# Optimization experiments

Hardware: AMD Instinct MI355X
Metric: run time of the kernel (lower is better)

## Reference

```python
import jax, jax.numpy as jnp
import numpy as np

B, L, D, H = 2, 256, 256, 4
DH = D // H  # 64


def setup_inputs() -> dict:
    key = jax.random.key(0)
    ks = jax.random.split(key, 20)
    inp = {
        "q": jax.random.normal(ks[0], (B, L, D), jnp.float32),
        "k": jax.random.normal(ks[1], (B, L, D), jnp.float32),
        "v": jax.random.normal(ks[2], (B, L, D), jnp.float32),
        "attn_mask": jnp.zeros((L, L), jnp.float32),  # nonzero => masked
        "key_padding_mask": jnp.zeros((B, L), bool),
        "pitch_rel": jax.random.normal(ks[3], (B, L, L, D), jnp.float32),
        "dur_rel": jax.random.normal(ks[4], (B, L, L, D), jnp.float32),
    }
    scale = 1.0 / np.sqrt(D)
    names = ["Wq", "Wk", "Wv", "fc", "pr", "dr"]
    for i, n in enumerate(names):
        inp[n + "_w"] = jax.random.normal(ks[5 + 2 * i], (D, D), jnp.float32) * scale
        inp[n + "_b"] = jax.random.normal(ks[6 + 2 * i], (D,), jnp.float32) * 0.01
    return inp


def _linear(x, w, b):
    # torch nn.Linear: y = x @ W^T + b
    return jnp.matmul(x, w.T) + b


def reference(q, k, v, attn_mask, key_padding_mask, pitch_rel, dur_rel,
              Wq_w, Wq_b, Wk_w, Wk_b, Wv_w, Wv_b, fc_w, fc_b,
              pr_w, pr_b, dr_w, dr_b):
    Bq, Lq, Dm = q.shape
    Lk = k.shape[1]
    # project and split heads -> (B, H, L, DH)
    def heads(x, w, b):
        return _linear(x, w, b).reshape(Bq, -1, H, DH).transpose(0, 2, 1, 3)
    qh, kh, vh = heads(q, Wq_w, Wq_b), heads(k, Wk_w, Wk_b), heads(v, Wv_w, Wv_b)

    # content scores: (B, H, Lq, Lk)
    logits = jnp.einsum("bhid,bhjd->bhij", qh, kh)

    # relative pitch bias: pitch_rel (B, Lq, Lk, D) -> (B, Lq, Lk, H, DH)
    pr = _linear(pitch_rel, pr_w, pr_b).reshape(Bq, Lq, Lk, H, DH)
    logits = logits + jnp.einsum("bhid,bijhd->bhij", qh, pr)

    dr = _linear(dur_rel, dr_w, dr_b).reshape(Bq, Lq, Lk, H, DH)
    logits = logits + jnp.einsum("bhid,bijhd->bhij", qh, dr)

    logits = logits / np.sqrt(DH)

    # mask: key_padding_mask broadcast over the QUERY axis (as in source),
    # attn_mask nonzero => masked
    mask = jnp.logical_or(key_padding_mask[:, None, :, None],
                          (attn_mask != 0)[None, None, :, :])
    logits = jnp.where(mask, jnp.float32(-9e15), logits)

    attn = jax.nn.softmax(logits, axis=-1)  # (B, H, Lq, Lk)
    out = jnp.einsum("bhij,bhjd->bhid", attn, vh)  # (B, H, Lq, DH)
    out = out.transpose(0, 2, 1, 3).reshape(Bq, Lq, Dm)
    out = _linear(out, fc_w, fc_b)  # dropout is identity in eval mode
    return out, attn
```

## Files before the change

kernel.cpp:

```cpp
#include <hip/hip_runtime.h>
#include <math.h>


__global__ __launch_bounds__(256) void k_transpose(const float* __restrict__ in,
                                                   float* __restrict__ out) {
  __shared__ float t[32][33];
  int bx = blockIdx.x & 7, by = blockIdx.x >> 3;
  int x = threadIdx.x & 31, y0 = threadIdx.x >> 5;
#pragma unroll
  for (int yy = 0; yy < 32; yy += 8)
    t[yy + y0][x] = in[(size_t)(by * 32 + yy + y0) * 256 + bx * 32 + x];
  __syncthreads();
#pragma unroll
  for (int yy = 0; yy < 32; yy += 8)
    out[(size_t)(bx * 32 + yy + y0) * 256 + by * 32 + x] = t[x][yy + y0];
}

__global__ __launch_bounds__(256) void k_proj(
    const float* __restrict__ q, const float* __restrict__ k_, const float* __restrict__ v,
    const float* __restrict__ Wq, const float* __restrict__ Bq,
    const float* __restrict__ Wk, const float* __restrict__ Bk,
    const float* __restrict__ Wv, const float* __restrict__ Bv,
    float* __restrict__ qh, float* __restrict__ kh, float* __restrict__ vh) {
  int blk = blockIdx.x;
  int m = blk >> 5;
  int r = blk & 31;
  int b = r >> 4, it = (r >> 2) & 3, ot = r & 3;
  const float* X = (m == 0) ? q : (m == 1) ? k_ : v;
  const float* W = (m == 0) ? Wq : (m == 1) ? Wk : Wv;
  const float* Bs = (m == 0) ? Bq : (m == 1) ? Bk : Bv;
  float* OUT = (m == 0) ? qh : (m == 1) ? kh : vh;
  const float scale = (m == 0) ? 0.125f : 1.0f;

  __shared__ float xs[64][33];
  __shared__ float ws[64][33];
  int tid = threadIdx.x;
  int ti = tid >> 4, to = tid & 15;
  int lr = tid >> 2, lc = (tid & 3) * 8;
  float acc[4][4] = {};

  for (int k0 = 0; k0 < 256; k0 += 32) {
    float4 a0 = *(const float4*)(X + (size_t)(b * 256 + it * 64 + lr) * 256 + k0 + lc);
    float4 a1 = *(const float4*)(X + (size_t)(b * 256 + it * 64 + lr) * 256 + k0 + lc + 4);
    xs[lr][lc + 0] = a0.x; xs[lr][lc + 1] = a0.y; xs[lr][lc + 2] = a0.z; xs[lr][lc + 3] = a0.w;
    xs[lr][lc + 4] = a1.x; xs[lr][lc + 5] = a1.y; xs[lr][lc + 6] = a1.z; xs[lr][lc + 7] = a1.w;
    float4 w0 = *(const float4*)(W + (size_t)(ot * 64 + lr) * 256 + k0 + lc);
    float4 w1 = *(const float4*)(W + (size_t)(ot * 64 + lr) * 256 + k0 + lc + 4);
    ws[lr][lc + 0] = w0.x; ws[lr][lc + 1] = w0.y; ws[lr][lc + 2] = w0.z; ws[lr][lc + 3] = w0.w;
    ws[lr][lc + 4] = w1.x; ws[lr][lc + 5] = w1.y; ws[lr][lc + 6] = w1.z; ws[lr][lc + 7] = w1.w;
    __syncthreads();
#pragma unroll
    for (int kk = 0; kk < 32; ++kk) {
      float xv0 = xs[ti * 4 + 0][kk], xv1 = xs[ti * 4 + 1][kk];
      float xv2 = xs[ti * 4 + 2][kk], xv3 = xs[ti * 4 + 3][kk];
      float wv0 = ws[0 * 16 + to][kk], wv1 = ws[1 * 16 + to][kk];
      float wv2 = ws[2 * 16 + to][kk], wv3 = ws[3 * 16 + to][kk];
      acc[0][0] += xv0 * wv0; acc[0][1] += xv0 * wv1; acc[0][2] += xv0 * wv2; acc[0][3] += xv0 * wv3;
      acc[1][0] += xv1 * wv0; acc[1][1] += xv1 * wv1; acc[1][2] += xv1 * wv2; acc[1][3] += xv1 * wv3;
      acc[2][0] += xv2 * wv0; acc[2][1] += xv2 * wv1; acc[2][2] += xv2 * wv2; acc[2][3] += xv2 * wv3;
      acc[3][0] += xv3 * wv0; acc[3][1] += xv3 * wv1; acc[3][2] += xv3 * wv2; acc[3][3] += xv3 * wv3;
    }
    __syncthreads();
  }
#pragma unroll
  for (int ii = 0; ii < 4; ++ii)
#pragma unroll
    for (int oo = 0; oo < 4; ++oo) {
      int i = it * 64 + ti * 4 + ii;
      int dd = oo * 16 + to;
      OUT[(size_t)((b * 4 + ot) * 256 + i) * 64 + dd] = (acc[ii][oo] + Bs[ot * 64 + dd]) * scale;
    }
}

__global__ __launch_bounds__(256) void k_qprdr(
    const float* __restrict__ qh, const float* __restrict__ prw,
    const float* __restrict__ drw, float* __restrict__ qpr, float* __restrict__ qdr) {
  int blk = blockIdx.x;
  int t = blk >> 7;
  int r2 = blk & 127;
  int rt = r2 >> 2, et = r2 & 3;
  const float* W = t ? drw : prw;
  float* OUT = t ? qdr : qpr;
  int h = (rt >> 2) & 3;

  __shared__ float xs[64][33];
  __shared__ float ws2[32][64];
  int tid = threadIdx.x;
  int ti = tid >> 4, to = tid & 15;
  float acc[4][4] = {};

  for (int k0 = 0; k0 < 64; k0 += 32) {
    int lr = tid >> 2, lc = (tid & 3) * 8;
    float4 a0 = *(const float4*)(qh + (size_t)(rt * 64 + lr) * 64 + k0 + lc);
    float4 a1 = *(const float4*)(qh + (size_t)(rt * 64 + lr) * 64 + k0 + lc + 4);
    xs[lr][lc + 0] = a0.x; xs[lr][lc + 1] = a0.y; xs[lr][lc + 2] = a0.z; xs[lr][lc + 3] = a0.w;
    xs[lr][lc + 4] = a1.x; xs[lr][lc + 5] = a1.y; xs[lr][lc + 6] = a1.z; xs[lr][lc + 7] = a1.w;
    int wr = tid >> 3, wc = (tid & 7) * 8;
    float4 w0 = *(const float4*)(W + (size_t)(h * 64 + k0 + wr) * 256 + et * 64 + wc);
    float4 w1 = *(const float4*)(W + (size_t)(h * 64 + k0 + wr) * 256 + et * 64 + wc + 4);
    ws2[wr][wc + 0] = w0.x; ws2[wr][wc + 1] = w0.y; ws2[wr][wc + 2] = w0.z; ws2[wr][wc + 3] = w0.w;
    ws2[wr][wc + 4] = w1.x; ws2[wr][wc + 5] = w1.y; ws2[wr][wc + 6] = w1.z; ws2[wr][wc + 7] = w1.w;
    __syncthreads();
#pragma unroll
    for (int kk = 0; kk < 32; ++kk) {
      float xv0 = xs[ti * 4 + 0][kk], xv1 = xs[ti * 4 + 1][kk];
      float xv2 = xs[ti * 4 + 2][kk], xv3 = xs[ti * 4 + 3][kk];
      float wv0 = ws2[kk][0 * 16 + to], wv1 = ws2[kk][1 * 16 + to];
      float wv2 = ws2[kk][2 * 16 + to], wv3 = ws2[kk][3 * 16 + to];
      acc[0][0] += xv0 * wv0; acc[0][1] += xv0 * wv1; acc[0][2] += xv0 * wv2; acc[0][3] += xv0 * wv3;
      acc[1][0] += xv1 * wv0; acc[1][1] += xv1 * wv1; acc[1][2] += xv1 * wv2; acc[1][3] += xv1 * wv3;
      acc[2][0] += xv2 * wv0; acc[2][1] += xv2 * wv1; acc[2][2] += xv2 * wv2; acc[2][3] += xv2 * wv3;
      acc[3][0] += xv3 * wv0; acc[3][1] += xv3 * wv1; acc[3][2] += xv3 * wv2; acc[3][3] += xv3 * wv3;
    }
    __syncthreads();
  }
#pragma unroll
  for (int ii = 0; ii < 4; ++ii)
#pragma unroll
    for (int oo = 0; oo < 4; ++oo)
      OUT[(size_t)(rt * 64 + ti * 4 + ii) * 256 + et * 64 + oo * 16 + to] = acc[ii][oo];
}

__global__ __launch_bounds__(256) void k_qk(const float* __restrict__ qh,
                                            const float* __restrict__ kh,
                                            float* __restrict__ qk) {
  int blk = blockIdx.x;
  int bh = blk >> 4, it = (blk >> 2) & 3, jt = blk & 3;
  __shared__ float xs[64][33];
  __shared__ float ys[64][33];
  int tid = threadIdx.x;
  int ti = tid >> 4, to = tid & 15;
  float acc[4][4] = {};

  for (int k0 = 0; k0 < 64; k0 += 32) {
    int lr = tid >> 2, lc = (tid & 3) * 8;
    float4 a0 = *(const float4*)(qh + (size_t)(bh * 256 + it * 64 + lr) * 64 + k0 + lc);
    float4 a1 = *(const float4*)(qh + (size_t)(bh * 256 + it * 64 + lr) * 64 + k0 + lc + 4);
    xs[lr][lc + 0] = a0.x; xs[lr][lc + 1] = a0.y; xs[lr][lc + 2] = a0.z; xs[lr][lc + 3] = a0.w;
    xs[lr][lc + 4] = a1.x; xs[lr][lc + 5] = a1.y; xs[lr][lc + 6] = a1.z; xs[lr][lc + 7] = a1.w;
    float4 b0 = *(const float4*)(kh + (size_t)(bh * 256 + jt * 64 + lr) * 64 + k0 + lc);
    float4 b1 = *(const float4*)(kh + (size_t)(bh * 256 + jt * 64 + lr) * 64 + k0 + lc + 4);
    ys[lr][lc + 0] = b0.x; ys[lr][lc + 1] = b0.y; ys[lr][lc + 2] = b0.z; ys[lr][lc + 3] = b0.w;
    ys[lr][lc + 4] = b1.x; ys[lr][lc + 5] = b1.y; ys[lr][lc + 6] = b1.z; ys[lr][lc + 7] = b1.w;
    __syncthreads();
#pragma unroll
    for (int kk = 0; kk < 32; ++kk) {
      float xv0 = xs[ti * 4 + 0][kk], xv1 = xs[ti * 4 + 1][kk];
      float xv2 = xs[ti * 4 + 2][kk], xv3 = xs[ti * 4 + 3][kk];
      float wv0 = ys[0 * 16 + to][kk], wv1 = ys[1 * 16 + to][kk];
      float wv2 = ys[2 * 16 + to][kk], wv3 = ys[3 * 16 + to][kk];
      acc[0][0] += xv0 * wv0; acc[0][1] += xv0 * wv1; acc[0][2] += xv0 * wv2; acc[0][3] += xv0 * wv3;
      acc[1][0] += xv1 * wv0; acc[1][1] += xv1 * wv1; acc[1][2] += xv1 * wv2; acc[1][3] += xv1 * wv3;
      acc[2][0] += xv2 * wv0; acc[2][1] += xv2 * wv1; acc[2][2] += xv2 * wv2; acc[2][3] += xv2 * wv3;
      acc[3][0] += xv3 * wv0; acc[3][1] += xv3 * wv1; acc[3][2] += xv3 * wv2; acc[3][3] += xv3 * wv3;
    }
    __syncthreads();
  }
#pragma unroll
  for (int ii = 0; ii < 4; ++ii)
#pragma unroll
    for (int jj = 0; jj < 4; ++jj)
      qk[(size_t)(bh * 256 + it * 64 + ti * 4 + ii) * 256 + jt * 64 + jj * 16 + to] = acc[ii][jj];
}

__global__ __launch_bounds__(256, 3) void k_bias(
    const float* __restrict__ pitch, const float* __restrict__ dur,
    const float* __restrict__ qpr, const float* __restrict__ qdr,
    const float* __restrict__ amask, const unsigned char* __restrict__ kpm,
    float* __restrict__ attn) {
  int blk = blockIdx.x;
  int jc = blk & 7;
  int bi = blk >> 3;
  int b = bi >> 8, i = bi & 255;
  int tid = threadIdx.x, w = tid >> 6, l = tid & 63;
  int jb = jc * 32 + w * 8;

  __shared__ float red[4][8][4][65];

  float4 qp[4], qd[4];
#pragma unroll
  for (int h = 0; h < 4; ++h) {
    qp[h] = *(const float4*)(qpr + (size_t)((b * 4 + h) * 256 + i) * 256 + 4 * l);
    qd[h] = *(const float4*)(qdr + (size_t)((b * 4 + h) * 256 + i) * 256 + 4 * l);
  }

  int p = l & 31;
  int jj_o = p >> 2, h_o = p & 3;
  int jabs = jb + jj_o;
  size_t orow = (size_t)((b * 4 + h_o) * 256 + i) * 256 + jabs;
  float qkreg = attn[orow];
  bool maskreg = (kpm[b * 256 + i] != 0) || (amask[(size_t)i * 256 + jabs] != 0.f);

  const float4* prow = (const float4*)(pitch + ((size_t)(b * 256 + i) * 256 + jb) * 256);
  const float4* drow = (const float4*)(dur + ((size_t)(b * 256 + i) * 256 + jb) * 256);

  float4 P[8], D[8];
#pragma unroll
  for (int g = 0; g < 8; ++g) P[g] = prow[(size_t)g * 64 + l];
#pragma unroll
  for (int g = 0; g < 8; ++g) D[g] = drow[(size_t)g * 64 + l];

  float acc[8][4];
#pragma unroll
  for (int jj = 0; jj < 8; ++jj)
#pragma unroll
    for (int h = 0; h < 4; ++h)
      acc[jj][h] = P[jj].x * qp[h].x + P[jj].y * qp[h].y + P[jj].z * qp[h].z + P[jj].w * qp[h].w
                 + D[jj].x * qd[h].x + D[jj].y * qd[h].y + D[jj].z * qd[h].z + D[jj].w * qd[h].w;

#pragma unroll
  for (int jj = 0; jj < 8; ++jj)
#pragma unroll
    for (int h = 0; h < 4; ++h)
      red[w][jj][h][l] = acc[jj][h];

  int half = l >> 5;
  const float* rrow = &red[w][jj_o][h_o][0];
  float x = 0.f;
#pragma unroll
  for (int c = 0; c < 32; ++c) x += rrow[half * 32 + c];
  x += __shfl_xor(x, 32);

  if (l < 32) {
    float val = qkreg + x;
    if (maskreg) val = -9e15f;
    attn[orow] = val;
  }
}

__global__ __launch_bounds__(256) void k_pv_fc(
    float* __restrict__ attn, const float* __restrict__ vh,
    const float* __restrict__ fcT, const float* __restrict__ fcb,
    float* __restrict__ out) {
  int b = blockIdx.x >> 8, i = blockIdx.x & 255;
  int tid = threadIdx.x;
  int h = tid >> 6, l = tid & 63;

  __shared__ float arow[4][256];
  __shared__ float pre[256];

  float* rowp = attn + (size_t)((b * 4 + h) * 256 + i) * 256;
  float4 v4 = *(float4*)(rowp + 4 * l);
  float mx = fmaxf(fmaxf(v4.x, v4.y), fmaxf(v4.z, v4.w));
#pragma unroll
  for (int m = 1; m <= 32; m <<= 1) mx = fmaxf(mx, __shfl_xor(mx, m));
  float e0 = __expf(v4.x - mx), e1 = __expf(v4.y - mx);
  float e2 = __expf(v4.z - mx), e3 = __expf(v4.w - mx);
  float sm = e0 + e1 + e2 + e3;
#pragma unroll
  for (int m = 1; m <= 32; m <<= 1) sm += __shfl_xor(sm, m);
  float inv = 1.0f / sm;
  float4 a4 = make_float4(e0 * inv, e1 * inv, e2 * inv, e3 * inv);
  *(float4*)(rowp + 4 * l) = a4;
  *(float4*)&arow[h][4 * l] = a4;
  __syncthreads();

  float acc = 0.f;
  const float* vbase = vh + (size_t)(b * 4 + h) * 256 * 64 + l;
#pragma unroll 4
  for (int jj = 0; jj < 256; ++jj) acc += arow[h][jj] * vbase[(size_t)jj * 64];
  pre[tid] = acc;
  __syncthreads();

  float acc2 = fcb[tid];
#pragma unroll 4
  for (int c = 0; c < 256; ++c) acc2 += pre[c] * fcT[(size_t)c * 256 + tid];
  out[(size_t)(b * 256 + i) * 256 + tid] = acc2;
}

extern "C" void kernel_launch(void* const* d_in, const int* in_sizes, int n_in,
                              void* d_out, int out_size, void* d_ws, size_t ws_size,
                              hipStream_t stream) {
  (void)in_sizes; (void)n_in; (void)out_size; (void)ws_size;
  const float* q = (const float*)d_in[0];
  const float* k = (const float*)d_in[1];
  const float* v = (const float*)d_in[2];
  const float* amask = (const float*)d_in[3];
  const unsigned char* kpm = (const unsigned char*)d_in[4];
  const float* pitch = (const float*)d_in[5];
  const float* dur = (const float*)d_in[6];
  const float* Wq = (const float*)d_in[7];
  const float* Bq = (const float*)d_in[8];
  const float* Wk = (const float*)d_in[9];
  const float* Bk = (const float*)d_in[10];
  const float* Wv = (const float*)d_in[11];
  const float* Bv = (const float*)d_in[12];
  const float* fcw = (const float*)d_in[13];
  const float* fcb = (const float*)d_in[14];
  const float* prw = (const float*)d_in[15];
  const float* drw = (const float*)d_in[17];

  float* out = (float*)d_out;
  float* attn = out + 2 * 256 * 256;

  float* wsf = (float*)d_ws;
  float* qh = wsf;
  float* kh = qh + 131072;
  float* vh = kh + 131072;
  float* qpr = vh + 131072;
  float* qdr = qpr + 524288;
  float* fcT = qdr + 524288;

  k_transpose<<<64, 256, 0, stream>>>(fcw, fcT);
  k_proj<<<96, 256, 0, stream>>>(q, k, v, Wq, Bq, Wk, Bk, Wv, Bv, qh, kh, vh);
  k_qprdr<<<256, 256, 0, stream>>>(qh, prw, drw, qpr, qdr);
  k_qk<<<128, 256, 0, stream>>>(qh, kh, attn);
  k_bias<<<4096, 256, 0, stream>>>(pitch, dur, qpr, qdr, amask, kpm, attn);
  k_pv_fc<<<512, 256, 0, stream>>>(attn, vh, fcT, fcb, out);
}
```

Measured before the change: 117.0 us.

## Double-buffer pitch/dur loads in k_bias with one block per query row

The relative-bias kernel now gives each block a whole query row, so each wave covers 64 keys in 8 groups instead of one group of 8 keys. Register loads for the next group are issued before the current group is reduced and stored, overlapping memory traffic with compute. The large pitch/dur streams are read with nontemporal loads to avoid polluting the cache. The grid shrinks from 4096 to 512 blocks and the launch bound drops to 2 blocks per unit, trading occupancy for more registers and in-wave latency hiding.

```diff
diff --git a/kernel.cpp b/kernel.cpp
--- a/kernel.cpp
+++ b/kernel.cpp
@@ -1,6 +1,13 @@
 #include <hip/hip_runtime.h>
 #include <math.h>
 
+
+typedef float nfloat4 __attribute__((ext_vector_type(4)));
+
+static __device__ __forceinline__ float4 ntload4(const float4* p) {
+  nfloat4 r = __builtin_nontemporal_load((const nfloat4*)p);
+  return make_float4(r.x, r.y, r.z, r.w);
+}
 
 __global__ __launch_bounds__(256) void k_transpose(const float* __restrict__ in,
                                                    float* __restrict__ out) {
@@ -163,17 +170,15 @@
       qk[(size_t)(bh * 256 + it * 64 + ti * 4 + ii) * 256 + jt * 64 + jj * 16 + to] = acc[ii][jj];
 }
 
-__global__ __launch_bounds__(256, 3) void k_bias(
+__global__ __launch_bounds__(256, 2) void k_bias(
     const float* __restrict__ pitch, const float* __restrict__ dur,
     const float* __restrict__ qpr, const float* __restrict__ qdr,
     const float* __restrict__ amask, const unsigned char* __restrict__ kpm,
     float* __restrict__ attn) {
-  int blk = blockIdx.x;
-  int jc = blk & 7;
-  int bi = blk >> 3;
+  int bi = blockIdx.x;
   int b = bi >> 8, i = bi & 255;
   int tid = threadIdx.x, w = tid >> 6, l = tid & 63;
-  int jb = jc * 32 + w * 8;
+  int jbase = w * 64;
 
   __shared__ float red[4][8][4][65];
 
@@ -186,46 +191,64 @@
 
   int p = l & 31;
   int jj_o = p >> 2, h_o = p & 3;
-  int jabs = jb + jj_o;
-  size_t orow = (size_t)((b * 4 + h_o) * 256 + i) * 256 + jabs;
-  float qkreg = attn[orow];
-  bool maskreg = (kpm[b * 256 + i] != 0) || (amask[(size_t)i * 256 + jabs] != 0.f);
-
-  const float4* prow = (const float4*)(pitch + ((size_t)(b * 256 + i) * 256 + jb) * 256);
-  const float4* drow = (const float4*)(dur + ((size_t)(b * 256 + i) * 256 + jb) * 256);
-
-  float4 P[8], D[8];
-#pragma unroll
-  for (int g = 0; g < 8; ++g) P[g] = prow[(size_t)g * 64 + l];
-#pragma unroll
-  for (int g = 0; g < 8; ++g) D[g] = drow[(size_t)g * 64 + l];
-
-  float acc[8][4];
-#pragma unroll
-  for (int jj = 0; jj < 8; ++jj)
-#pragma unroll
-    for (int h = 0; h < 4; ++h)
-      acc[jj][h] = P[jj].x * qp[h].x + P[jj].y * qp[h].y + P[jj].z * qp[h].z + P[jj].w * qp[h].w
-                 + D[jj].x * qd[h].x + D[jj].y * qd[h].y + D[jj].z * qd[h].z + D[jj].w * qd[h].w;
-
-#pragma unroll
-  for (int jj = 0; jj < 8; ++jj)
-#pragma unroll
-    for (int h = 0; h < 4; ++h)
-      red[w][jj][h][l] = acc[jj][h];
-
-  int half = l >> 5;
-  const float* rrow = &red[w][jj_o][h_o][0];
-  float x = 0.f;
-#pragma unroll
-  for (int c = 0; c < 32; ++c) x += rrow[half * 32 + c];
-  x += __shfl_xor(x, 32);
-
-  if (l < 32) {
-    float val = qkreg + x;
-    if (maskreg) val = -9e15f;
-    attn[orow] = val;
-  }
+  size_t orow0 = (size_t)((b * 4 + h_o) * 256 + i) * 256 + jbase + jj_o;
+  bool rowm = kpm[b * 256 + i] != 0;
+  float qk8[8];
+  int mbits = 0;
+#pragma unroll
+  for (int g = 0; g < 8; ++g) {
+    qk8[g] = attn[orow0 + 8 * g];
+    if (rowm || amask[(size_t)i * 256 + jbase + g * 8 + jj_o] != 0.f) mbits |= (1 << g);
+  }
+
+  const float4* prow =
+      (const float4*)(pitch + (size_t)(b * 256 + i) * 65536) + (size_t)jbase * 64 + l;
+  const float4* drow =
+      (const float4*)(dur + (size_t)(b * 256 + i) * 65536) + (size_t)jbase * 64 + l;
+
+  float4 Pa[8], Da[8], Pb[8], Db[8];
+
+#define LOADG(PB, DB, g)                                  \
+  {                                                       \
+    _Pragma("unroll") for (int t = 0; t < 8; ++t) {       \
+      PB[t] = ntload4(prow + ((g) * 8 + t) * 64);         \
+      DB[t] = ntload4(drow + ((g) * 8 + t) * 64);         \
+    }                                                     \
+  }
+
+#define CSTORE(PB, DB, g)                                                       \
+  {                                                                             \
+    _Pragma("unroll") for (int t = 0; t < 8; ++t) {                             \
+      _Pragma("unroll") for (int h = 0; h < 4; ++h) {                           \
+        red[w][t][h][l] =                                                       \
+            PB[t].x * qp[h].x + PB[t].y * qp[h].y + PB[t].z * qp[h].z +         \
+            PB[t].w * qp[h].w + DB[t].x * qd[h].x + DB[t].y * qd[h].y +         \
+            DB[t].z * qd[h].z + DB[t].w * qd[h].w;                              \
+      }                                                                         \
+    }                                                                           \
+    float x = 0.f;                                                              \
+    {                                                                           \
+      const float* rr = &red[w][jj_o][h_o][(l >> 5) * 32];                      \
+      _Pragma("unroll 8") for (int c = 0; c < 32; ++c) x += rr[c];              \
+    }                                                                           \
+    x += __shfl_xor(x, 32);                                                     \
+    if (l < 32) {                                                               \
+      float val = qk8[g] + x;                                                   \
+      if (mbits & (1 << (g))) val = -9e15f;                                     \
+      attn[orow0 + 8 * (g)] = val;                                              \
+    }                                                                           \
+  }
+
+  LOADG(Pa, Da, 0);
+#pragma unroll
+  for (int gg = 0; gg < 4; ++gg) {
+    LOADG(Pb, Db, 2 * gg + 1);
+    CSTORE(Pa, Da, 2 * gg);
+    if (gg < 3) LOADG(Pa, Da, 2 * gg + 2);
+    CSTORE(Pb, Db, 2 * gg + 1);
+  }
+#undef LOADG
+#undef CSTORE
 }
 
 __global__ __launch_bounds__(256) void k_pv_fc(
@@ -305,6 +328,6 @@
   k_proj<<<96, 256, 0, stream>>>(q, k, v, Wq, Bq, Wk, Bk, Wv, Bv, qh, kh, vh);
   k_qprdr<<<256, 256, 0, stream>>>(qh, prw, drw, qpr, qdr);
   k_qk<<<128, 256, 0, stream>>>(qh, kh, attn);
-  k_bias<<<4096, 256, 0, stream>>>(pitch, dur, qpr, qdr, amask, kpm, attn);
+  k_bias<<<512, 256, 0, stream>>>(pitch, dur, qpr, qdr, amask, kpm, attn);
   k_pv_fc<<<512, 256, 0, stream>>>(attn, vh, fcT, fcb, out);
 }
```

New measurement: 120.7 us. 1.03x slower.

## Merge small kernels, restructure bias kernel for occupancy, move masking into softmax

Applied to the files above, without the earlier changes.

The transpose, q·pr/q·dr and QK kernels are folded into one launch that dispatches on block index, removing two launches. The bias kernel now writes the pitch/duration bias to a separate workspace buffer. It processes 64 keys per block in four groups, uses fewer registers and a smaller shared-memory reduction, and is bounded for 8 blocks per CU instead of 3. The QK add, masking and softmax are folded into the PV+FC kernel. The bias kernel keeps fewer loads in flight per thread in exchange for higher occupancy, and the new bias buffer adds an extra global write and read.

```diff
diff --git a/kernel.cpp b/kernel.cpp
--- a/kernel.cpp
+++ b/kernel.cpp
@@ -1,20 +1,6 @@
 #include <hip/hip_runtime.h>
 #include <math.h>
 
-
-__global__ __launch_bounds__(256) void k_transpose(const float* __restrict__ in,
-                                                   float* __restrict__ out) {
-  __shared__ float t[32][33];
-  int bx = blockIdx.x & 7, by = blockIdx.x >> 3;
-  int x = threadIdx.x & 31, y0 = threadIdx.x >> 5;
-#pragma unroll
-  for (int yy = 0; yy < 32; yy += 8)
-    t[yy + y0][x] = in[(size_t)(by * 32 + yy + y0) * 256 + bx * 32 + x];
-  __syncthreads();
-#pragma unroll
-  for (int yy = 0; yy < 32; yy += 8)
-    out[(size_t)(bx * 32 + yy + y0) * 256 + by * 32 + x] = t[x][yy + y0];
-}
 
 __global__ __launch_bounds__(256) void k_proj(
     const float* __restrict__ q, const float* __restrict__ k_, const float* __restrict__ v,
@@ -72,10 +58,9 @@
     }
 }
 
-__global__ __launch_bounds__(256) void k_qprdr(
-    const float* __restrict__ qh, const float* __restrict__ prw,
-    const float* __restrict__ drw, float* __restrict__ qpr, float* __restrict__ qdr) {
-  int blk = blockIdx.x;
+static __device__ void body_qprdr(int blk, const float* __restrict__ qh,
+                                  const float* __restrict__ prw, const float* __restrict__ drw,
+                                  float* __restrict__ qpr, float* __restrict__ qdr) {
   int t = blk >> 7;
   int r2 = blk & 127;
   int rt = r2 >> 2, et = r2 & 3;
@@ -121,10 +106,8 @@
       OUT[(size_t)(rt * 64 + ti * 4 + ii) * 256 + et * 64 + oo * 16 + to] = acc[ii][oo];
 }
 
-__global__ __launch_bounds__(256) void k_qk(const float* __restrict__ qh,
-                                            const float* __restrict__ kh,
-                                            float* __restrict__ qk) {
-  int blk = blockIdx.x;
+static __device__ void body_qk(int blk, const float* __restrict__ qh,
+                               const float* __restrict__ kh, float* __restrict__ qk) {
   int bh = blk >> 4, it = (blk >> 2) & 3, jt = blk & 3;
   __shared__ float xs[64][33];
   __shared__ float ys[64][33];
@@ -163,19 +146,43 @@
       qk[(size_t)(bh * 256 + it * 64 + ti * 4 + ii) * 256 + jt * 64 + jj * 16 + to] = acc[ii][jj];
 }
 
-__global__ __launch_bounds__(256, 3) void k_bias(
+static __device__ void body_transpose(int blk, const float* __restrict__ in,
+                                      float* __restrict__ out) {
+  __shared__ float t[32][33];
+  int bx = blk & 7, by = blk >> 3;
+  int x = threadIdx.x & 31, y0 = threadIdx.x >> 5;
+#pragma unroll
+  for (int yy = 0; yy < 32; yy += 8)
+    t[yy + y0][x] = in[(size_t)(by * 32 + yy + y0) * 256 + bx * 32 + x];
+  __syncthreads();
+#pragma unroll
+  for (int yy = 0; yy < 32; yy += 8)
+    out[(size_t)(bx * 32 + yy + y0) * 256 + by * 32 + x] = t[x][yy + y0];
+}
+
+__global__ __launch_bounds__(256) void k_mid(
+    const float* __restrict__ qh, const float* __restrict__ kh,
+    const float* __restrict__ prw, const float* __restrict__ drw,
+    float* __restrict__ qpr, float* __restrict__ qdr, float* __restrict__ qk,
+    const float* __restrict__ fcw, float* __restrict__ fcT) {
+  int blk = blockIdx.x;
+  if (blk < 256) body_qprdr(blk, qh, prw, drw, qpr, qdr);
+  else if (blk < 384) body_qk(blk - 256, qh, kh, qk);
+  else body_transpose(blk - 384, fcw, fcT);
+}
+
+__global__ __launch_bounds__(256, 8) void k_bias(
     const float* __restrict__ pitch, const float* __restrict__ dur,
     const float* __restrict__ qpr, const float* __restrict__ qdr,
-    const float* __restrict__ amask, const unsigned char* __restrict__ kpm,
-    float* __restrict__ attn) {
+    float* __restrict__ bias) {
   int blk = blockIdx.x;
-  int jc = blk & 7;
-  int bi = blk >> 3;
+  int jc = blk & 3;
+  int bi = blk >> 2;
   int b = bi >> 8, i = bi & 255;
   int tid = threadIdx.x, w = tid >> 6, l = tid & 63;
-  int jb = jc * 32 + w * 8;
-
-  __shared__ float red[4][8][4][65];
+  int j0 = jc * 64 + w * 16;
+
+  __shared__ float red[4][4][4][65];
 
   float4 qp[4], qd[4];
 #pragma unroll
@@ -184,54 +191,44 @@
     qd[h] = *(const float4*)(qdr + (size_t)((b * 4 + h) * 256 + i) * 256 + 4 * l);
   }
 
-  int p = l & 31;
-  int jj_o = p >> 2, h_o = p & 3;
-  int jabs = jb + jj_o;
-  size_t orow = (size_t)((b * 4 + h_o) * 256 + i) * 256 + jabs;
-  float qkreg = attn[orow];
-  bool maskreg = (kpm[b * 256 + i] != 0) || (amask[(size_t)i * 256 + jabs] != 0.f);
-
-  const float4* prow = (const float4*)(pitch + ((size_t)(b * 256 + i) * 256 + jb) * 256);
-  const float4* drow = (const float4*)(dur + ((size_t)(b * 256 + i) * 256 + jb) * 256);
-
-  float4 P[8], D[8];
-#pragma unroll
-  for (int g = 0; g < 8; ++g) P[g] = prow[(size_t)g * 64 + l];
-#pragma unroll
-  for (int g = 0; g < 8; ++g) D[g] = drow[(size_t)g * 64 + l];
-
-  float acc[8][4];
-#pragma unroll
-  for (int jj = 0; jj < 8; ++jj)
-#pragma unroll
-    for (int h = 0; h < 4; ++h)
-      acc[jj][h] = P[jj].x * qp[h].x + P[jj].y * qp[h].y + P[jj].z * qp[h].z + P[jj].w * qp[h].w
-                 + D[jj].x * qd[h].x + D[jj].y * qd[h].y + D[jj].z * qd[h].z + D[jj].w * qd[h].w;
-
-#pragma unroll
-  for (int jj = 0; jj < 8; ++jj)
-#pragma unroll
-    for (int h = 0; h < 4; ++h)
-      red[w][jj][h][l] = acc[jj][h];
-
-  int half = l >> 5;
-  const float* rrow = &red[w][jj_o][h_o][0];
-  float x = 0.f;
-#pragma unroll
-  for (int c = 0; c < 32; ++c) x += rrow[half * 32 + c];
-  x += __shfl_xor(x, 32);
-
-  if (l < 32) {
-    float val = qkreg + x;
-    if (maskreg) val = -9e15f;
-    attn[orow] = val;
-  }
-}
-
-__global__ __launch_bounds__(256) void k_pv_fc(
-    float* __restrict__ attn, const float* __restrict__ vh,
+  int p2 = l & 15, row_o = p2 >> 2, h_o = p2 & 3, sub = l >> 4;
+  size_t obase = ((size_t)(b * 4 + h_o) * 256 + i) * 256 + j0 + row_o;
+
+  const float* pbase = pitch + ((size_t)bi * 256 + j0) * 256 + 4 * l;
+  const float* dbase = dur + ((size_t)bi * 256 + j0) * 256 + 4 * l;
+
+#pragma unroll
+  for (int g = 0; g < 4; ++g) {
+#pragma unroll
+    for (int r = 0; r < 4; ++r) {
+      float4 P = *(const float4*)(pbase + (g * 4 + r) * 256);
+      float4 Dv = *(const float4*)(dbase + (g * 4 + r) * 256);
+      red[w][r][0][l] = P.x * qp[0].x + P.y * qp[0].y + P.z * qp[0].z + P.w * qp[0].w
+                      + Dv.x * qd[0].x + Dv.y * qd[0].y + Dv.z * qd[0].z + Dv.w * qd[0].w;
+      red[w][r][1][l] = P.x * qp[1].x + P.y * qp[1].y + P.z * qp[1].z + P.w * qp[1].w
+                      + Dv.x * qd[1].x + Dv.y * qd[1].y + Dv.z * qd[1].z + Dv.w * qd[1].w;
+      red[w][r][2][l] = P.x * qp[2].x + P.y * qp[2].y + P.z * qp[2].z + P.w * qp[2].w
+                      + Dv.x * qd[2].x + Dv.y * qd[2].y + Dv.z * qd[2].z + Dv.w * qd[2].w;
+      red[w][r][3][l] = P.x * qp[3].x + P.y * qp[3].y + P.z * qp[3].z + P.w * qp[3].w
+                      + Dv.x * qd[3].x + Dv.y * qd[3].y + Dv.z * qd[3].z + Dv.w * qd[3].w;
+    }
+    float x = 0.f;
+    {
+      const float* rr = &red[w][row_o][h_o][sub * 16];
+#pragma unroll
+      for (int c = 0; c < 16; ++c) x += rr[c];
+    }
+    x += __shfl_xor(x, 16);
+    x += __shfl_xor(x, 32);
+    if (l < 16) bias[obase + g * 4] = x;
+  }
+}
+
+__global__ __launch_bounds__(256) void k_pvfc(
+    const float* __restrict__ bias, const float* __restrict__ amask,
+    const unsigned char* __restrict__ kpm, const float* __restrict__ vh,
     const float* __restrict__ fcT, const float* __restrict__ fcb,
-    float* __restrict__ out) {
+    float* __restrict__ attn, float* __restrict__ out) {
   int b = blockIdx.x >> 8, i = blockIdx.x & 255;
   int tid = threadIdx.x;
   int h = tid >> 6, l = tid & 63;
@@ -239,21 +236,29 @@
   __shared__ float arow[4][256];
   __shared__ float pre[256];
 
-  float* rowp = attn + (size_t)((b * 4 + h) * 256 + i) * 256;
-  float4 v4 = *(float4*)(rowp + 4 * l);
-  float mx = fmaxf(fmaxf(v4.x, v4.y), fmaxf(v4.z, v4.w));
+  bool rowm = kpm[b * 256 + i] != 0;
+  float* qrow = attn + (size_t)((b * 4 + h) * 256 + i) * 256;
+  const float* brow = bias + (size_t)((b * 4 + h) * 256 + i) * 256;
+  float4 v4 = *(float4*)(qrow + 4 * l);
+  float4 b4 = *(const float4*)(brow + 4 * l);
+  float4 m4 = *(const float4*)(amask + (size_t)i * 256 + 4 * l);
+  float v0 = (rowm || m4.x != 0.f) ? -9e15f : v4.x + b4.x;
+  float v1 = (rowm || m4.y != 0.f) ? -9e15f : v4.y + b4.y;
+  float v2 = (rowm || m4.z != 0.f) ? -9e15f : v4.z + b4.z;
+  float v3 = (rowm || m4.w != 0.f) ? -9e15f : v4.w + b4.w;
+
+  float mx = fmaxf(fmaxf(v0, v1), fmaxf(v2, v3));
 #pragma unroll
   for (int m = 1; m <= 32; m <<= 1) mx = fmaxf(mx, __shfl_xor(mx, m));
-  float e0 = __expf(v4.x - mx), e1 = __expf(v4.y - mx);
-  float e2 = __expf(v4.z - mx), e3 = __expf(v4.w - mx);
+  float e0 = __expf(v0 - mx), e1 = __expf(v1 - mx);
+  float e2 = __expf(v2 - mx), e3 = __expf(v3 - mx);
   float sm = e0 + e1 + e2 + e3;
 #pragma unroll
   for (int m = 1; m <= 32; m <<= 1) sm += __shfl_xor(sm, m);
   float inv = 1.0f / sm;
   float4 a4 = make_float4(e0 * inv, e1 * inv, e2 * inv, e3 * inv);
-  *(float4*)(rowp + 4 * l) = a4;
+  *(float4*)(qrow + 4 * l) = a4;
   *(float4*)&arow[h][4 * l] = a4;
-  __syncthreads();
 
   float acc = 0.f;
   const float* vbase = vh + (size_t)(b * 4 + h) * 256 * 64 + l;
@@ -300,11 +305,10 @@
   float* qpr = vh + 131072;
   float* qdr = qpr + 524288;
   float* fcT = qdr + 524288;
-
-  k_transpose<<<64, 256, 0, stream>>>(fcw, fcT);
+  float* bias = fcT + 65536;
+
   k_proj<<<96, 256, 0, stream>>>(q, k, v, Wq, Bq, Wk, Bk, Wv, Bv, qh, kh, vh);
-  k_qprdr<<<256, 256, 0, stream>>>(qh, prw, drw, qpr, qdr);
-  k_qk<<<128, 256, 0, stream>>>(qh, kh, attn);
-  k_bias<<<4096, 256, 0, stream>>>(pitch, dur, qpr, qdr, amask, kpm, attn);
-  k_pv_fc<<<512, 256, 0, stream>>>(attn, vh, fcT, fcb, out);
-}
+  k_mid<<<448, 256, 0, stream>>>(qh, kh, prw, drw, qpr, qdr, attn, fcw, fcT);
+  k_bias<<<2048, 256, 0, stream>>>(pitch, dur, qpr, qdr, bias);
+  k_pvfc<<<512, 256, 0, stream>>>(bias, amask, kpm, vh, fcT, fcb, attn, out);
+}
```

Result: faster. 114.5 us (-2.1%).
